# Performance work log

Hardware: AMD Instinct MI355X
Metric: run time of the kernel (lower is better)

## Reference

```python
import jax, jax.numpy as jnp
import numpy as np

D = 1024
H = 16
HD = D // H
B = 2
T = 2048


def setup_inputs() -> dict:
    key = jax.random.key(0)
    ks = jax.random.split(key, 5)
    x = jax.random.normal(ks[0], (B, T, D), dtype=jnp.float32)
    # PyTorch SDPA bool-mask semantics: True = attend. Causal lower-triangular.
    attn_mask = jnp.tril(jnp.ones((T, T), dtype=bool))
    w_qkv = jax.random.normal(ks[1], (3 * D, D), dtype=jnp.float32) * (1.0 / np.sqrt(D))
    b_qkv = jax.random.normal(ks[2], (3 * D,), dtype=jnp.float32) * 0.02
    w_proj = jax.random.normal(ks[3], (D, D), dtype=jnp.float32) * (1.0 / np.sqrt(D))
    b_proj = jax.random.normal(ks[4], (D,), dtype=jnp.float32) * 0.02
    return {"x": x, "attn_mask": attn_mask, "w_qkv": w_qkv, "b_qkv": b_qkv,
            "w_proj": w_proj, "b_proj": b_proj}


def reference(x, attn_mask, w_qkv, b_qkv, w_proj, b_proj):
    b, t, d = x.shape
    # fused QKV projection (torch Linear: y = x @ W.T + b)
    qkv = jnp.einsum('btd,ed->bte', x, w_qkv) + b_qkv  # [B,T,3D]
    q, k, v = jnp.split(qkv, 3, axis=-1)
    # [B,T,D] -> [B,H,T,hd]
    def heads(z):
        return z.reshape(b, t, H, HD).transpose(0, 2, 1, 3)
    q, k, v = heads(q), heads(k), heads(v)
    scale = 1.0 / jnp.sqrt(jnp.asarray(HD, dtype=x.dtype))
    scores = jnp.einsum('bhqd,bhkd->bhqk', q, k) * scale  # [B,H,T,T]
    neg_inf = jnp.asarray(jnp.finfo(x.dtype).min, dtype=x.dtype)
    scores = jnp.where(attn_mask, scores, neg_inf)
    attn = jax.nn.softmax(scores, axis=-1)
    y = jnp.einsum('bhqk,bhkd->bhqd', attn, v)  # [B,H,T,hd]
    y = y.transpose(0, 2, 1, 3).reshape(b, t, d)
    y = jnp.einsum('btd,ed->bte', y, w_proj) + b_proj
    return y
```

## Files before the change

kernel.cpp:

```cpp
#include <hip/hip_runtime.h>
#include <hip/hip_bf16.h>
#include <math.h>

#define D_MODEL 1024
#define NHEAD   16
#define HDIM    64
#define BATCH   2
#define SEQ     2048
#define MTOT    (BATCH * SEQ)

typedef unsigned short u16;
typedef unsigned int u32;
typedef short short8 __attribute__((ext_vector_type(8)));
typedef float floatx4 __attribute__((ext_vector_type(4)));

#define LOG2E 1.44269504088896340736f
#define QSCALE 0.18033688011112042f

#if __has_builtin(__builtin_amdgcn_exp2f)
#define EXP2(x) __builtin_amdgcn_exp2f(x)
#else
#define EXP2(x) exp2f(x)
#endif

static __device__ __forceinline__ u16 f2b(float f) {
  union { __hip_bfloat16 h; u16 u; } cv;
  cv.h = __float2bfloat16(f);
  return cv.u;
}

typedef const __attribute__((address_space(1))) unsigned int guint;
typedef __attribute__((address_space(3))) unsigned int luint;
static __device__ __forceinline__ void gl_lds16(const u16* g, u16* l) {
  __builtin_amdgcn_global_load_lds((guint*)g, (luint*)l, 16, 0, 0);
}

__global__ __launch_bounds__(256) void cast3_f2b(
    const float* __restrict__ a, u16* __restrict__ ao, int na,
    const float* __restrict__ b, u16* __restrict__ bo, int nb,
    const float* __restrict__ c, u16* __restrict__ co) {
  int i = (blockIdx.x * 256 + threadIdx.x) * 4;
  const float* src;
  u16* dst;
  if (i < na) {
    src = a + i;
    dst = ao + i;
  } else if (i < na + nb) {
    src = b + (i - na);
    dst = bo + (i - na);
  } else {
    src = c + (i - na - nb);
    dst = co + (i - na - nb);
  }
  float4 v = *(const float4*)src;
  ushort4 o;
  o.x = f2b(v.x);
  o.y = f2b(v.y);
  o.z = f2b(v.z);
  o.w = f2b(v.w);
  *(ushort4*)dst = o;
}

template <int MODE, int AR>
__global__ __launch_bounds__(256) void gemm_bt_bf16(
    const u16* __restrict__ A, const u16* __restrict__ Bm,
    const float* __restrict__ bias, u16* __restrict__ Cq, u16* __restrict__ Ck,
    u16* __restrict__ Cvt, float* __restrict__ Cf, int M, int N, int K) {
  constexpr int MI = AR / 32;
  constexpr int SMREQ = 2 * (AR + 128) * 32;
  constexpr int SM = (MODE == 0) ? (SMREQ > 17408 ? SMREQ : 17408) : SMREQ;
  __shared__ u16 smem[SM];
  u16(*As)[AR][32] = (u16(*)[AR][32])smem;
  u16(*Bs)[128][32] = (u16(*)[128][32])(smem + 2 * AR * 32);

  const int tid = threadIdx.x;
  const int lane = tid & 63;
  const int wave = tid >> 6;
  const int wm = (wave >> 1) * (AR / 2);
  const int wn = (wave & 1) * 64;
  const int quad = lane >> 4;
  const int l15 = lane & 15;

  const int flat = blockIdx.x + gridDim.x * blockIdx.y;
  const int xcd = flat & 7;
  const int local = flat >> 3;
  const int mr = gridDim.y >> 3;
  const int m0 = (xcd * mr + (local % mr)) * AR;
  const int n0 = (local / mr) * 128;

  const int srow = wave * 16 + (lane >> 2);
  const int k8 = (lane & 3) * 8;

  const u16* gA0 = A + (size_t)(m0 + srow) * K + k8;
  const u16* gA1 = A + (size_t)(m0 + srow + 64) * K + k8;
  const u16* gB0 = Bm + (size_t)(n0 + srow) * K + k8;
  const u16* gB1 = Bm + (size_t)(n0 + srow + 64) * K + k8;

  floatx4 acc[MI][4];
#pragma unroll
  for (int i = 0; i < MI; ++i)
#pragma unroll
    for (int j = 0; j < 4; ++j)
#pragma unroll
      for (int e = 0; e < 4; ++e) acc[i][j][e] = 0.0f;

  gl_lds16(gA0, &As[0][srow][k8]);
  if (AR == 128) gl_lds16(gA1, &As[0][srow + 64][k8]);
  gl_lds16(gB0, &Bs[0][srow][k8]);
  gl_lds16(gB1, &Bs[0][srow + 64][k8]);

  const int niter = K / 32;
  for (int kt = 0; kt < niter; ++kt) {
    const int cur = kt & 1;
    __syncthreads();
    if (kt + 1 < niter) {
      const int k0n = (kt + 1) * 32;
      gl_lds16(gA0 + k0n, &As[cur ^ 1][srow][k8]);
      if (AR == 128) gl_lds16(gA1 + k0n, &As[cur ^ 1][srow + 64][k8]);
      gl_lds16(gB0 + k0n, &Bs[cur ^ 1][srow][k8]);
      gl_lds16(gB1 + k0n, &Bs[cur ^ 1][srow + 64][k8]);
    }
    short8 af[MI], bf[4];
#pragma unroll
    for (int i = 0; i < MI; ++i)
      af[i] = *(const short8*)&As[cur][wm + i * 16 + l15][quad * 8];
#pragma unroll
    for (int j = 0; j < 4; ++j)
      bf[j] = *(const short8*)&Bs[cur][wn + j * 16 + l15][quad * 8];
#pragma unroll
    for (int i = 0; i < MI; ++i)
#pragma unroll
      for (int j = 0; j < 4; ++j)
        acc[i][j] = __builtin_amdgcn_mfma_f32_16x16x32_bf16(af[i], bf[j],
                                                            acc[i][j], 0, 0, 0);
  }

  if (MODE == 0) {
    const int nbase = n0 + wn;
    const int sel = nbase >> 10;
    const int h = (nbase >> 6) & (NHEAD - 1);
    if (sel == 2) {
      __syncthreads();
      u16(*Vs)[68] = (u16(*)[68])(smem + wave * 4352);
#pragma unroll
      for (int j = 0; j < 4; ++j) {
        const float bv = bias[nbase + j * 16 + l15];
        const int d = j * 16 + l15;
#pragma unroll
        for (int i = 0; i < MI; ++i) {
          ushort4 o4;
          o4.x = f2b(acc[i][j][0] + bv);
          o4.y = f2b(acc[i][j][1] + bv);
          o4.z = f2b(acc[i][j][2] + bv);
          o4.w = f2b(acc[i][j][3] + bv);
          *(ushort4*)&Vs[d][i * 16 + quad * 4] = o4;
        }
      }
      const int mb0 = m0 + wm;
      const int b = mb0 >> 11;
      const int t0 = mb0 & (SEQ - 1);
      u16* vbase = Cvt + ((size_t)(b * NHEAD + h) * HDIM) * SEQ + t0;
      const int dl = lane >> 3;
      const int t8 = (lane & 7) * 8;
#pragma unroll
      for (int p = 0; p < 8; ++p) {
        const int d = p * 8 + dl;
        *(short8*)(vbase + (size_t)d * SEQ + t8) = *(const short8*)&Vs[d][t8];
      }
    } else {
      u16* dst = (sel == 0) ? Cq : Ck;
      const float qsc = (sel == 0) ? QSCALE : 1.0f;
      __syncthreads();
      u16(*Ct)[68] = (u16(*)[68])(smem + wave * 4352);
#pragma unroll
      for (int j = 0; j < 4; ++j) {
        const float bv = bias[nbase + j * 16 + l15];
#pragma unroll
        for (int i = 0; i < MI; ++i)
#pragma unroll
          for (int r = 0; r < 4; ++r)
            Ct[i * 16 + quad * 4 + r][j * 16 + l15] =
                f2b((acc[i][j][r] + bv) * qsc);
      }
      const int mb0 = m0 + wm;
      const int b = mb0 >> 11;
      const int t0 = mb0 & (SEQ - 1);
      u16* rowbase = dst + ((size_t)(b * NHEAD + h) * SEQ + t0) * HDIM;
      const int tr = lane >> 3;
      const int d8 = (lane & 7) * 8;
#pragma unroll
      for (int p = 0; p < 8; ++p) {
        const int row = p * 8 + tr;
        *(short8*)(rowbase + (size_t)row * HDIM + d8) =
            *(const short8*)&Ct[row][d8];
      }
    }
  } else {
#pragma unroll
    for (int j = 0; j < 4; ++j) {
      const int n = n0 + wn + j * 16 + l15;
      const float bv = bias[n];
#pragma unroll
      for (int i = 0; i < MI; ++i) {
        const int mb = m0 + wm + i * 16 + quad * 4;
#pragma unroll
        for (int r = 0; r < 4; ++r)
          Cf[(size_t)(mb + r) * N + n] = acc[i][j][r] + bv;
      }
    }
  }
}

__global__ __launch_bounds__(256) void flash_mfma(const u16* __restrict__ Qg,
                                                  const u16* __restrict__ Kg,
                                                  const u16* __restrict__ Vtg,
                                                  u16* __restrict__ Yb) {
  __shared__ u16 Ks[2][64][76];
  __shared__ u16 Vt[2][64][76];
  __shared__ u16 Pb[64][76];

  const int tid = threadIdx.x;
  const int lane = tid & 63;
  const int wave = tid >> 6;
  const int wrow = wave * 16;
  const int quad = lane >> 4;
  const int l15 = lane & 15;
  const int bh = blockIdx.y;
  const int b = bh >> 4;
  const int h = bh & (NHEAD - 1);

  const u16* Qp = Qg + (size_t)bh * SEQ * HDIM;
  const u16* Kp = Kg + (size_t)bh * SEQ * HDIM;
  const u16* Vp = Vtg + (size_t)bh * HDIM * SEQ;

  const int srow = tid >> 2;
  const int sc = (tid & 3) * 16;

#pragma unroll
  for (int phase = 0; phase < 2; ++phase) {
    const int qt = phase == 0 ? (16 + blockIdx.x) : (15 - blockIdx.x);
    const int q0 = qt * 64;

    __syncthreads();

    short8 aq[2];
    {
      const u16* qrow = Qp + (size_t)(q0 + wrow + l15) * HDIM + quad * 8;
      aq[0] = *(const short8*)qrow;
      aq[1] = *(const short8*)(qrow + 32);
    }

    floatx4 o[4];
#pragma unroll
    for (int c = 0; c < 4; ++c)
#pragma unroll
      for (int e = 0; e < 4; ++e) o[c][e] = 0.0f;
    float l_acc[4] = {0.0f, 0.0f, 0.0f, 0.0f};

    const int nkt = qt + 1;
    short8 kv0 = *(const short8*)(Kp + (size_t)srow * HDIM + sc);
    short8 kv1 = *(const short8*)(Kp + (size_t)srow * HDIM + sc + 8);
    short8 vv0 = *(const short8*)(Vp + (size_t)srow * SEQ + sc);
    short8 vv1 = *(const short8*)(Vp + (size_t)srow * SEQ + sc + 8);

    for (int kt = 0; kt < nkt; ++kt) {
      const int k0 = kt * 64;
      const int buf = kt & 1;
      *(short8*)&Ks[buf][srow][sc] = kv0;
      *(short8*)&Ks[buf][srow][sc + 8] = kv1;
      *(short8*)&Vt[buf][srow][sc] = vv0;
      *(short8*)&Vt[buf][srow][sc + 8] = vv1;
      __syncthreads();
      if (kt + 1 < nkt) {
        const u16* kp = Kp + (size_t)(k0 + 64 + srow) * HDIM + sc;
        const u16* vp = Vp + (size_t)srow * SEQ + k0 + 64 + sc;
        kv0 = *(const short8*)kp;
        kv1 = *(const short8*)(kp + 8);
        vv0 = *(const short8*)vp;
        vv1 = *(const short8*)(vp + 8);
      }

      short8 bk[4][2];
#pragma unroll
      for (int c = 0; c < 4; ++c)
#pragma unroll
        for (int kk = 0; kk < 2; ++kk)
          bk[c][kk] =
              *(const short8*)&Ks[buf][c * 16 + l15][kk * 32 + quad * 8];

      floatx4 s[4];
#pragma unroll
      for (int c = 0; c < 4; ++c) {
#pragma unroll
        for (int e = 0; e < 4; ++e) s[c][e] = 0.0f;
        s[c] = __builtin_amdgcn_mfma_f32_16x16x32_bf16(aq[0], bk[c][0], s[c],
                                                       0, 0, 0);
        s[c] = __builtin_amdgcn_mfma_f32_16x16x32_bf16(aq[1], bk[c][1], s[c],
                                                       0, 0, 0);
      }

      const bool msk = (kt == nkt - 1);
      const int prow = wrow + quad * 4;
#pragma unroll
      for (int c = 0; c < 4; ++c)
#pragma unroll
        for (int r = 0; r < 4; ++r) {
          float p = EXP2(s[c][r]);
          if (msk) {
            const int row = q0 + prow + r;
            const int col = k0 + c * 16 + l15;
            if (col > row) p = 0.0f;
          }
          l_acc[r] += p;
          Pb[prow + r][c * 16 + l15] = f2b(p);
        }

      short8 ap[2];
#pragma unroll
      for (int kk = 0; kk < 2; ++kk)
        ap[kk] = *(const short8*)&Pb[wrow + l15][kk * 32 + quad * 8];
#pragma unroll
      for (int c = 0; c < 4; ++c) {
        short8 bv0 = *(const short8*)&Vt[buf][c * 16 + l15][quad * 8];
        short8 bv1 = *(const short8*)&Vt[buf][c * 16 + l15][32 + quad * 8];
        o[c] = __builtin_amdgcn_mfma_f32_16x16x32_bf16(ap[0], bv0, o[c], 0, 0,
                                                       0);
        o[c] = __builtin_amdgcn_mfma_f32_16x16x32_bf16(ap[1], bv1, o[c], 0, 0,
                                                       0);
      }
    }

#pragma unroll
    for (int r = 0; r < 4; ++r) {
      l_acc[r] += __shfl_xor(l_acc[r], 1);
      l_acc[r] += __shfl_xor(l_acc[r], 2);
      l_acc[r] += __shfl_xor(l_acc[r], 4);
      l_acc[r] += __shfl_xor(l_acc[r], 8);
    }

#pragma unroll
    for (int r = 0; r < 4; ++r) {
      const float inv = 1.0f / l_acc[r];
      const int t = q0 + wrow + quad * 4 + r;
#pragma unroll
      for (int c = 0; c < 4; ++c)
        Yb[((size_t)b * SEQ + t) * D_MODEL + h * HDIM + c * 16 + l15] =
            f2b(o[c][r] * inv);
    }
  }
}

extern "C" void kernel_launch(void* const* d_in, const int* in_sizes, int n_in,
                              void* d_out, int out_size, void* d_ws,
                              size_t ws_size, hipStream_t stream) {
  const float* x = (const float*)d_in[0];
  const float* w_qkv = (const float*)d_in[2];
  const float* b_qkv = (const float*)d_in[3];
  const float* w_proj = (const float*)d_in[4];
  const float* b_proj = (const float*)d_in[5];
  float* out = (float*)d_out;

  const size_t nx = (size_t)MTOT * D_MODEL;
  const size_t nwq = (size_t)3 * D_MODEL * D_MODEL;
  const size_t nwp = (size_t)D_MODEL * D_MODEL;
  const size_t nqkv = (size_t)BATCH * NHEAD * SEQ * HDIM;

  u16* xb = (u16*)d_ws;
  u16* wqb = xb + nx;
  u16* wpb = wqb + nwq;
  u16* qb = wpb + nwp;
  u16* kb = qb + nqkv;
  u16* vtb = kb + nqkv;
  u16* yb = vtb + nqkv;

  cast3_f2b<<<dim3((nx + nwq + nwp) / 1024), dim3(256), 0, stream>>>(
      x, xb, (int)nx, w_qkv, wqb, (int)nwq, w_proj, wpb);

  gemm_bt_bf16<0, 128><<<dim3(24, 32), dim3(256), 0, stream>>>(
      xb, wqb, b_qkv, qb, kb, vtb, nullptr, MTOT, 3 * D_MODEL, D_MODEL);
  flash_mfma<<<dim3(16, BATCH * NHEAD), dim3(256), 0, stream>>>(qb, kb, vtb,
                                                                yb);
  gemm_bt_bf16<1, 64><<<dim3(8, 64), dim3(256), 0, stream>>>(
      yb, wpb, b_proj, nullptr, nullptr, nullptr, out, MTOT, D_MODEL, D_MODEL);
}
```

Before: 184.2 us.

## Stage K/V tiles via direct global-to-LDS loads with XOR-swizzled layout

Replaces the register-staged K/V tile copy with direct global-to-LDS loads (gl_lds16) issued one tile ahead. The unpadded 64-wide LDS rows are laid out with an XOR swizzle, which keeps bank conflicts down on the MFMA operand reads. The intent is to cut VGPR pressure and the extra LDS-store instructions, and to overlap the next tile's fetch with compute. It relies on gl_lds16 being defined earlier and on a correct wait and barrier for the async loads; without that wait there is a risk of reading stale data.

```diff
diff --git a/kernel.cpp b/kernel.cpp
--- a/kernel.cpp
+++ b/kernel.cpp
@@ -215,8 +215,8 @@
                                                   const u16* __restrict__ Kg,
                                                   const u16* __restrict__ Vtg,
                                                   u16* __restrict__ Yb) {
-  __shared__ u16 Ks[2][64][76];
-  __shared__ u16 Vt[2][64][76];
+  __shared__ u16 Ks[2][64][64];
+  __shared__ u16 Vt[2][64][64];
   __shared__ u16 Pb[64][76];
 
   const int tid = threadIdx.x;
@@ -233,15 +233,32 @@
   const u16* Kp = Kg + (size_t)bh * SEQ * HDIM;
   const u16* Vp = Vtg + (size_t)bh * HDIM * SEQ;
 
-  const int srow = tid >> 2;
-  const int sc = (tid & 3) * 16;
+  const int gr = tid >> 3;
+  const int gg = tid & 7;
+  const int sg = (gg ^ (gr & 7)) << 3;
+  const int rsw = l15 & 7;
+
+  auto stage = [&](int b2, int k0s) {
+    const u16* kp0 = Kp + (size_t)(k0s + gr) * HDIM + sg;
+    const u16* kp1 = Kp + (size_t)(k0s + 32 + gr) * HDIM + sg;
+    const u16* vp0 = Vp + (size_t)gr * SEQ + k0s + sg;
+    const u16* vp1 = Vp + (size_t)(32 + gr) * SEQ + k0s + sg;
+    u16* kd = &Ks[b2][0][0] + (size_t)tid * 8;
+    u16* vd = &Vt[b2][0][0] + (size_t)tid * 8;
+    gl_lds16(kp0, kd);
+    gl_lds16(kp1, kd + 2048);
+    gl_lds16(vp0, vd);
+    gl_lds16(vp1, vd + 2048);
+  };
 
 #pragma unroll
   for (int phase = 0; phase < 2; ++phase) {
     const int qt = phase == 0 ? (16 + blockIdx.x) : (15 - blockIdx.x);
     const int q0 = qt * 64;
+    const int nkt = qt + 1;
 
     __syncthreads();
+    stage(0, 0);
 
     short8 aq[2];
     {
@@ -257,36 +274,19 @@
       for (int e = 0; e < 4; ++e) o[c][e] = 0.0f;
     float l_acc[4] = {0.0f, 0.0f, 0.0f, 0.0f};
 
-    const int nkt = qt + 1;
-    short8 kv0 = *(const short8*)(Kp + (size_t)srow * HDIM + sc);
-    short8 kv1 = *(const short8*)(Kp + (size_t)srow * HDIM + sc + 8);
-    short8 vv0 = *(const short8*)(Vp + (size_t)srow * SEQ + sc);
-    short8 vv1 = *(const short8*)(Vp + (size_t)srow * SEQ + sc + 8);
-
     for (int kt = 0; kt < nkt; ++kt) {
       const int k0 = kt * 64;
       const int buf = kt & 1;
-      *(short8*)&Ks[buf][srow][sc] = kv0;
-      *(short8*)&Ks[buf][srow][sc + 8] = kv1;
-      *(short8*)&Vt[buf][srow][sc] = vv0;
-      *(short8*)&Vt[buf][srow][sc + 8] = vv1;
       __syncthreads();
-      if (kt + 1 < nkt) {
-        const u16* kp = Kp + (size_t)(k0 + 64 + srow) * HDIM + sc;
-        const u16* vp = Vp + (size_t)srow * SEQ + k0 + 64 + sc;
-        kv0 = *(const short8*)kp;
-        kv1 = *(const short8*)(kp + 8);
-        vv0 = *(const short8*)vp;
-        vv1 = *(const short8*)(vp + 8);
-      }
+      if (kt + 1 < nkt) stage(buf ^ 1, k0 + 64);
 
       short8 bk[4][2];
 #pragma unroll
       for (int c = 0; c < 4; ++c)
 #pragma unroll
         for (int kk = 0; kk < 2; ++kk)
-          bk[c][kk] =
-              *(const short8*)&Ks[buf][c * 16 + l15][kk * 32 + quad * 8];
+          bk[c][kk] = *(const short8*)&Ks[buf][c * 16 + l15]
+                                         [(((kk << 2) + quad) ^ rsw) << 3];
 
       floatx4 s[4];
 #pragma unroll
@@ -321,8 +321,10 @@
         ap[kk] = *(const short8*)&Pb[wrow + l15][kk * 32 + quad * 8];
 #pragma unroll
       for (int c = 0; c < 4; ++c) {
-        short8 bv0 = *(const short8*)&Vt[buf][c * 16 + l15][quad * 8];
-        short8 bv1 = *(const short8*)&Vt[buf][c * 16 + l15][32 + quad * 8];
+        short8 bv0 =
+            *(const short8*)&Vt[buf][c * 16 + l15][(quad ^ rsw) << 3];
+        short8 bv1 =
+            *(const short8*)&Vt[buf][c * 16 + l15][((4 + quad) ^ rsw) << 3];
         o[c] = __builtin_amdgcn_mfma_f32_16x16x32_bf16(ap[0], bv0, o[c], 0, 0,
                                                        0);
         o[c] = __builtin_amdgcn_mfma_f32_16x16x32_bf16(ap[1], bv1, o[c], 0, 0,
```

After: 187.8 us. No clear change (+1.9%).

## Keep attention probabilities in registers via transposed S MFMA, skip masked tiles

Applied to the files above, without the earlier changes.

Computes S transposed (K as the A operand) so each lane's accumulator already holds the layout needed as the A operand of a 16x16x16 bf16 MFMA for P·V. This removes the Pb shared-memory round trip and its store/load traffic, and turns the row-sum reduction into two shuffles. On the diagonal tile, waves also skip key column blocks that lie entirely above the diagonal. In exchange, P·V uses twice as many smaller MFMAs, and V is read from LDS as narrower 4-element loads.

```diff
diff --git a/kernel.cpp b/kernel.cpp
--- a/kernel.cpp
+++ b/kernel.cpp
@@ -12,6 +12,7 @@
 typedef unsigned short u16;
 typedef unsigned int u32;
 typedef short short8 __attribute__((ext_vector_type(8)));
+typedef short short4v __attribute__((ext_vector_type(4)));
 typedef float floatx4 __attribute__((ext_vector_type(4)));
 
 #define LOG2E 1.44269504088896340736f
@@ -27,6 +28,18 @@
   union { __hip_bfloat16 h; u16 u; } cv;
   cv.h = __float2bfloat16(f);
   return cv.u;
+}
+
+static __device__ __forceinline__ floatx4 mfma16(short4v a, short4v b,
+                                                 floatx4 c) {
+#if __has_builtin(__builtin_amdgcn_mfma_f32_16x16x16bf16_1k)
+  return __builtin_amdgcn_mfma_f32_16x16x16bf16_1k(a, b, c, 0, 0, 0);
+#else
+  asm volatile("v_mfma_f32_16x16x16_bf16 %0, %1, %2, %0"
+               : "+v"(c)
+               : "v"(a), "v"(b));
+  return c;
+#endif
 }
 
 typedef const __attribute__((address_space(1))) unsigned int guint;
@@ -217,7 +230,6 @@
                                                   u16* __restrict__ Yb) {
   __shared__ u16 Ks[2][64][76];
   __shared__ u16 Vt[2][64][76];
-  __shared__ u16 Pb[64][76];
 
   const int tid = threadIdx.x;
   const int lane = tid & 63;
@@ -249,13 +261,14 @@
       aq[0] = *(const short8*)qrow;
       aq[1] = *(const short8*)(qrow + 32);
     }
+    const int qrowg = q0 + wrow + l15;
 
     floatx4 o[4];
 #pragma unroll
     for (int c = 0; c < 4; ++c)
 #pragma unroll
       for (int e = 0; e < 4; ++e) o[c][e] = 0.0f;
-    float l_acc[4] = {0.0f, 0.0f, 0.0f, 0.0f};
+    float l_acc = 0.0f;
 
     const int nkt = qt + 1;
     short8 kv0 = *(const short8*)(Kp + (size_t)srow * HDIM + sc);
@@ -280,67 +293,61 @@
         vv1 = *(const short8*)(vp + 8);
       }
 
-      short8 bk[4][2];
-#pragma unroll
-      for (int c = 0; c < 4; ++c)
-#pragma unroll
-        for (int kk = 0; kk < 2; ++kk)
-          bk[c][kk] =
-              *(const short8*)&Ks[buf][c * 16 + l15][kk * 32 + quad * 8];
+      const bool msk = (kt == nkt - 1);
 
       floatx4 s[4];
 #pragma unroll
       for (int c = 0; c < 4; ++c) {
-#pragma unroll
-        for (int e = 0; e < 4; ++e) s[c][e] = 0.0f;
-        s[c] = __builtin_amdgcn_mfma_f32_16x16x32_bf16(aq[0], bk[c][0], s[c],
-                                                       0, 0, 0);
-        s[c] = __builtin_amdgcn_mfma_f32_16x16x32_bf16(aq[1], bk[c][1], s[c],
-                                                       0, 0, 0);
-      }
-
-      const bool msk = (kt == nkt - 1);
-      const int prow = wrow + quad * 4;
-#pragma unroll
-      for (int c = 0; c < 4; ++c)
+        if (msk && c > wave) continue;
+        const u16* krow = &Ks[buf][c * 16 + l15][0];
+        const short8 bk0 = *(const short8*)(krow + quad * 8);
+        const short8 bk1 = *(const short8*)(krow + 32 + quad * 8);
+        floatx4 acc;
+#pragma unroll
+        for (int e = 0; e < 4; ++e) acc[e] = 0.0f;
+        acc = __builtin_amdgcn_mfma_f32_16x16x32_bf16(bk0, aq[0], acc, 0, 0,
+                                                      0);
+        acc = __builtin_amdgcn_mfma_f32_16x16x32_bf16(bk1, aq[1], acc, 0, 0,
+                                                      0);
+        s[c] = acc;
+      }
+
+      short4v pl[4];
+#pragma unroll
+      for (int c = 0; c < 4; ++c) {
+        if (msk && c > wave) continue;
+        const int kbase = k0 + c * 16 + quad * 4;
+        short4v pv;
 #pragma unroll
         for (int r = 0; r < 4; ++r) {
           float p = EXP2(s[c][r]);
-          if (msk) {
-            const int row = q0 + prow + r;
-            const int col = k0 + c * 16 + l15;
-            if (col > row) p = 0.0f;
-          }
-          l_acc[r] += p;
-          Pb[prow + r][c * 16 + l15] = f2b(p);
+          if (msk && (kbase + r > qrowg)) p = 0.0f;
+          l_acc += p;
+          pv[r] = (short)f2b(p);
         }
-
-      short8 ap[2];
-#pragma unroll
-      for (int kk = 0; kk < 2; ++kk)
-        ap[kk] = *(const short8*)&Pb[wrow + l15][kk * 32 + quad * 8];
+        pl[c] = pv;
+      }
+
 #pragma unroll
       for (int c = 0; c < 4; ++c) {
-        short8 bv0 = *(const short8*)&Vt[buf][c * 16 + l15][quad * 8];
-        short8 bv1 = *(const short8*)&Vt[buf][c * 16 + l15][32 + quad * 8];
-        o[c] = __builtin_amdgcn_mfma_f32_16x16x32_bf16(ap[0], bv0, o[c], 0, 0,
-                                                       0);
-        o[c] = __builtin_amdgcn_mfma_f32_16x16x32_bf16(ap[1], bv1, o[c], 0, 0,
-                                                       0);
-      }
-    }
+        if (msk && c > wave) continue;
+        short4v bv[4];
+#pragma unroll
+        for (int cd = 0; cd < 4; ++cd)
+          bv[cd] =
+              *(const short4v*)&Vt[buf][cd * 16 + l15][c * 16 + quad * 4];
+#pragma unroll
+        for (int cd = 0; cd < 4; ++cd) o[cd] = mfma16(pl[c], bv[cd], o[cd]);
+      }
+    }
+
+    l_acc += __shfl_xor(l_acc, 16);
+    l_acc += __shfl_xor(l_acc, 32);
 
 #pragma unroll
     for (int r = 0; r < 4; ++r) {
-      l_acc[r] += __shfl_xor(l_acc[r], 1);
-      l_acc[r] += __shfl_xor(l_acc[r], 2);
-      l_acc[r] += __shfl_xor(l_acc[r], 4);
-      l_acc[r] += __shfl_xor(l_acc[r], 8);
-    }
-
-#pragma unroll
-    for (int r = 0; r < 4; ++r) {
-      const float inv = 1.0f / l_acc[r];
+      const float lv = __shfl(l_acc, quad * 4 + r);
+      const float inv = 1.0f / lv;
       const int t = q0 + wrow + quad * 4 + r;
 #pragma unroll
       for (int c = 0; c < 4; ++c)
```

New measurement: 220.5 us. 19.7% more time.
